# Performance work log

Measured on AMD Instinct MI355X. Metric: run time of the kernel, lower is better.

Reference implementation:

```python
import jax, jax.numpy as jnp
import numpy as np

B, S, T = 256, 1024, 64

def setup_inputs() -> dict:
    key = jax.random.key(0)
    k1, k2, k3, k4, k5 = jax.random.split(key, 5)
    emissions = jax.random.normal(k1, (B, S, T), dtype=jnp.float32)
    tags = jax.random.randint(k2, (B, S), 0, T, dtype=jnp.int64)
    mask = jnp.ones((B, S), dtype=jnp.int32)
    transitions = jax.random.normal(k3, (T, T), dtype=jnp.float32) * 0.1
    start_transitions = jax.random.normal(k4, (T,), dtype=jnp.float32) * 0.1
    end_transitions = jax.random.normal(k5, (T,), dtype=jnp.float32) * 0.1
    return {"emissions": emissions, "tags": tags, "mask": mask,
            "transitions": transitions, "start_transitions": start_transitions,
            "end_transitions": end_transitions}


def _gold_score(emissions, tags, maskf, transitions, start_transitions, end_transitions):
    # emission score at each gold tag: [B, S]
    emit = jnp.take_along_axis(emissions, tags[:, :, None], axis=2)[:, :, 0]
    # transition score between consecutive gold tags: [B, S-1]
    trans = transitions[tags[:, :-1], tags[:, 1:]]
    score = start_transitions[tags[:, 0]] + emit[:, 0]
    score = score + jnp.sum((trans + emit[:, 1:]) * maskf[:, 1:], axis=1)
    last_pos = maskf.astype(jnp.int32).sum(axis=1) - 1           # [B]
    last_tags = jnp.take_along_axis(tags, last_pos[:, None], axis=1)[:, 0]
    return score + end_transitions[last_tags]


def _log_partition(emissions, maskf, transitions, start_transitions, end_transitions):
    alpha0 = start_transitions[None, :] + emissions[:, 0]        # [B, T]

    def step(alpha, xs):
        emit_t, m_t = xs                                         # [B, T], [B]
        # scores[b, i, j] = alpha[b, i] + transitions[i, j] + emit_t[b, j]
        scores = alpha[:, :, None] + transitions[None, :, :] + emit_t[:, None, :]
        new_alpha = jax.nn.logsumexp(scores, axis=1)             # [B, T]
        alpha = jnp.where(m_t[:, None] > 0, new_alpha, alpha)
        return alpha, None

    xs = (jnp.swapaxes(emissions[:, 1:], 0, 1), jnp.swapaxes(maskf[:, 1:], 0, 1))
    alpha, _ = jax.lax.scan(step, alpha0, xs)
    return jax.nn.logsumexp(alpha + end_transitions[None, :], axis=1)  # [B]


def reference(emissions, tags, mask, transitions, start_transitions, end_transitions):
    maskf = mask.astype(emissions.dtype)
    log_Z = _log_partition(emissions, maskf, transitions, start_transitions, end_transitions)
    score = _gold_score(emissions, tags, maskf, transitions, start_transitions, end_transitions)
    return jnp.mean(log_Z - score)
```

## Files before the change

### kernel.cpp

```cpp
#include <hip/hip_runtime.h>

#define Bn 256
#define Sn 1024
#define Tn 64
#define NCH 16
#define BURN 64
#define SLAB 4
#define RAWSTR 260
#define CROW 72
#define MROW 129
#define LN2 0.69314718055994531f
#define L7LN2 4.8520302639196169f

typedef __attribute__((ext_vector_type(8))) short short8;
typedef __attribute__((ext_vector_type(4))) float f32x4;

__device__ __forceinline__ unsigned short f2bf_rne(float f) {
  unsigned u = __float_as_uint(f);
  u = (u + 0x7fffu + ((u >> 16) & 1u)) >> 16;
  return (unsigned short)u;
}
__device__ __forceinline__ unsigned pk2(float hi, float lo) {
  return __builtin_amdgcn_perm(__float_as_uint(hi), __float_as_uint(lo), 0x07060302);
}
__device__ __forceinline__ unsigned pke(float a, float b) {
  return (unsigned)f2bf_rne(__expf(a - L7LN2)) |
         ((unsigned)f2bf_rne(__expf(b - L7LN2)) << 16);
}
__device__ __forceinline__ short8 cat4(uint2 a, uint2 b) {
  union { unsigned u[4]; short8 s; } x;
  x.u[0] = a.x; x.u[1] = a.y; x.u[2] = b.x; x.u[3] = b.y;
  return x.s;
}
__device__ __forceinline__ void gl_lds16(const void* src, void* dst) {
  __builtin_amdgcn_global_load_lds(
      (const __attribute__((address_space(1))) void*)src,
      (__attribute__((address_space(3))) void*)dst, 16, 0, 0);
}
__device__ __forceinline__ void gl_lds4(const void* src, void* dst) {
  __builtin_amdgcn_global_load_lds(
      (const __attribute__((address_space(1))) void*)src,
      (__attribute__((address_space(3))) void*)dst, 4, 0, 0);
}

__global__ __launch_bounds__(256, 1) void crf_scan(
    const float* __restrict__ em, const int* __restrict__ tags,
    const int* __restrict__ mask, const float* __restrict__ trans,
    const float* __restrict__ startt, const float* __restrict__ endt,
    float* __restrict__ wsL, float* __restrict__ wsGold,
    int* __restrict__ wsM, float* __restrict__ wsSE, float* __restrict__ wsA,
    int* __restrict__ cnt, float* __restrict__ out) {
  const int g = blockIdx.x & 15;
  const int c = blockIdx.x >> 4;
  const int Wc = (c == 0) ? 0 : BURN;
  const int Lc = (c == NCH - 1) ? 63 : 64;
  const int TOT = Wc + Lc;
  const int NSLAB = (TOT + SLAB - 1) / SLAB;
  const int t0 = 64 * c + 1;
  const int tstart = t0 - Wc;
  const int tid = threadIdx.x;
  const int wid = tid >> 6;
  const int lane = tid & 63;
  const int m = lane & 15;
  const int q = lane >> 4;
  const int mrow = 8 * (m >> 2) + (m & 3);

  __shared__ __align__(16) float rawS[4][16 * RAWSTR];
  __shared__ __align__(16) short convS[2][SLAB * 16 * CROW];
  __shared__ int maskL[16 * MROW];
  __shared__ int lastF;
  __shared__ float eend[64];
  __shared__ float rsum[4];

  short8 a00, a01, a10, a11, a20, a21, a30, a31;
  uint2 st0, st1, st2, st3;
  float Slog = 0.f;
  int K = 0, NL = 0;
  const f32x4 zero4 = {0.f, 0.f, 0.f, 0.f};

  auto issue_rows = [&](int s, int mm0, int mm1) {
    if (s >= NSLAB) return;
    float* dstb = rawS[s & 3];
    const int rem = TOT - 4 * s;
    if (rem >= SLAB) {
      for (int mm = mm0; mm < mm1; ++mm)
        gl_lds16(em + ((size_t)(16 * g + mm) * Sn + tstart + 4 * s) * 64 + lane * 4,
                 dstb + mm * RAWSTR);
    } else {
      for (int mm = mm0; mm < mm1; ++mm)
        for (int u = 0; u < rem; ++u)
          gl_lds4(em + ((size_t)(16 * g + mm) * Sn + tstart + 4 * s + u) * 64 + lane,
                  dstb + mm * RAWSTR + u * 64);
    }
  };
  auto conv_u = [&](const float* rp, short* cb, int mm, int base, int u) {
    float4 v0 = *(const float4*)(rp + u * 64 + 0);
    float4 v1 = *(const float4*)(rp + u * 64 + 4);
    float4 v2 = *(const float4*)(rp + u * 64 + 8);
    float4 v3 = *(const float4*)(rp + u * 64 + 12);
    uint4 o0, o1;
    o0.x = pke(v0.x, v0.y); o0.y = pke(v0.z, v0.w);
    o1.x = pke(v1.x, v1.y); o1.y = pke(v1.z, v1.w);
    o0.z = pke(v2.x, v2.y); o0.w = pke(v2.z, v2.w);
    o1.z = pke(v3.x, v3.y); o1.w = pke(v3.z, v3.w);
    short* cw = cb + (u * 16 + mm) * CROW + base;
    *(uint4*)(cw) = o0;
    *(uint4*)(cw + 16) = o1;
  };
  auto convert2 = [&](int s, int ua) {
    if (s >= NSLAB) return;
    const int mm = lane & 15, seg = lane >> 4;
    const float* rp = rawS[s & 3] + mm * RAWSTR + seg * 16;
    short* cb = convS[s & 1];
    const int base = (seg >> 1) * 32 + (seg & 1) * 8;
    conv_u(rp, cb, mm, base, ua);
    conv_u(rp, cb, mm, base, ua + 1);
  };

  if (wid == 0) {
#define LOADA(tm, kc, dst) { \
    _Pragma("unroll") for (int jj = 0; jj < 8; ++jj) { \
      int kk = kc * 32 + q * 8 + jj; \
      dst[jj] = (short)f2bf_rne(__expf(trans[kk * Tn + (32 * ((tm) >> 1) + 4 * ((tm) & 1) + mrow)])); \
    } }
    LOADA(0, 0, a00) LOADA(0, 1, a01) LOADA(1, 0, a10) LOADA(1, 1, a11)
    LOADA(2, 0, a20) LOADA(2, 1, a21) LOADA(3, 0, a30) LOADA(3, 1, a31)
#undef LOADA
    if (c == 0) {
#define INIT0(off, ss) { \
      float4 sv = *(const float4*)(startt + (off)); \
      float4 ev = *(const float4*)(em + (size_t)(16 * g + m) * Sn * Tn + (off)); \
      ss.x = (unsigned)f2bf_rne(__expf(sv.x + ev.x)) | \
             ((unsigned)f2bf_rne(__expf(sv.y + ev.y)) << 16); \
      ss.y = (unsigned)f2bf_rne(__expf(sv.z + ev.z)) | \
             ((unsigned)f2bf_rne(__expf(sv.w + ev.w)) << 16); }
      INIT0(8 * q, st0) INIT0(8 * q + 4, st1)
      INIT0(32 + 8 * q, st2) INIT0(36 + 8 * q, st3)
#undef INIT0
    } else {
      st0.x = 0x3F803F80u; st0.y = 0x3F803F80u; st1 = st0; st2 = st0; st3 = st0;
    }
  } else if (wid == 1) {
    issue_rows(0, 0, 6); issue_rows(1, 0, 6); issue_rows(2, 0, 6);
    asm volatile("s_waitcnt vmcnt(0)" ::: "memory");
  } else if (wid == 2) {
    issue_rows(0, 6, 12); issue_rows(1, 6, 12); issue_rows(2, 6, 12);
    const int bm = 16 * g + m;
    const int* tg = tags + (size_t)bm * Sn;
    const int* mkb = mask + (size_t)bm * Sn;
    const float* emb = em + (size_t)bm * Sn * Tn;
    float acc = 0.f;
    int cntg = 0;
    #pragma unroll 4
    for (int i = 0; i < 16; ++i) {
      int t = t0 + q + 4 * i;
      bool ok = t < t0 + Lc;
      int ts = ok ? t : t0;
      int mv = mkb[ts];
      int tp = tg[ts - 1], tc = tg[ts];
      float w = trans[tp * Tn + tc] + emb[(size_t)ts * Tn + tc];
      acc += (ok && mv) ? w : 0.f;
      cntg += ok ? mv : 0;
    }
    acc += __shfl_xor(acc, 16); acc += __shfl_xor(acc, 32);
    cntg += __shfl_xor(cntg, 16); cntg += __shfl_xor(cntg, 32);
    if (q == 0) { wsGold[c * 256 + bm] = acc; wsM[c * 256 + bm] = cntg; }
    asm volatile("s_waitcnt vmcnt(0)" ::: "memory");
  } else {
    issue_rows(0, 12, 16); issue_rows(1, 12, 16); issue_rows(2, 12, 16);
    for (int mm = 0; mm < 16; ++mm) {
      gl_lds4(mask + (size_t)(16 * g + mm) * Sn + tstart + lane,
              (void*)(maskL + mm * MROW));
      bool special = (c == NCH - 1) && (g == 15) && (mm == 15);
      if (!special)
        gl_lds4(mask + (size_t)(16 * g + mm) * Sn + tstart + 64 + lane,
                (void*)(maskL + mm * MROW + 64));
    }
    if (c == NCH - 1 && g == 15) {
      int t = tstart + 64 + lane;
      if (t < Sn) maskL[15 * MROW + 64 + lane] = mask[(size_t)255 * Sn + t];
    }
    asm volatile("s_waitcnt vmcnt(0) lgkmcnt(0)" ::: "memory");
  }
  __syncthreads();

  if (wid == 1) convert2(0, 0);
  else if (wid == 2) convert2(0, 2);
  __syncthreads();

#define UNP(ss, x0, x1, x2, x3) \
  x0 = __uint_as_float(ss.x << 16); x1 = __uint_as_float(ss.x & 0xffff0000u); \
  x2 = __uint_as_float(ss.y << 16); x3 = __uint_as_float(ss.y & 0xffff0000u);

  auto renorm = [&](int ttz) {
    float x00, x01, x02, x03, x10, x11, x12, x13;
    float x20, x21, x22, x23, x30, x31, x32, x33;
    UNP(st0, x00, x01, x02, x03) UNP(st1, x10, x11, x12, x13)
    UNP(st2, x20, x21, x22, x23) UNP(st3, x30, x31, x32, x33)
    float sm = (((x00 + x01) + (x02 + x03)) + ((x10 + x11) + (x12 + x13)))
             + (((x20 + x21) + (x22 + x23)) + ((x30 + x31) + (x32 + x33)));
    sm += __shfl_xor(sm, 16); sm += __shfl_xor(sm, 32);
    if (c != 0 && ttz == BURN) { Slog = __logf(sm); K = 0; NL = 0; }
    int k = 127 - (int)((__float_as_uint(sm) >> 23) & 255u);
    float fk = __uint_as_float((unsigned)(127 + k) << 23);
    x00 *= fk; x01 *= fk; x02 *= fk; x03 *= fk;
    x10 *= fk; x11 *= fk; x12 *= fk; x13 *= fk;
    x20 *= fk; x21 *= fk; x22 *= fk; x23 *= fk;
    x30 *= fk; x31 *= fk; x32 *= fk; x33 *= fk;
    st0.x = pk2(x01, x00); st0.y = pk2(x03, x02);
    st1.x = pk2(x11, x10); st1.y = pk2(x13, x12);
    st2.x = pk2(x21, x20); st2.y = pk2(x23, x22);
    st3.x = pk2(x31, x30); st3.y = pk2(x33, x32);
    K += k;
  };

  auto scan_step = [&](const short* ep, int tt) {
    uint2 eu0 = *(const uint2*)(ep + 0 + 4 * q);
    uint2 eu1 = *(const uint2*)(ep + 16 + 4 * q);
    uint2 eu2 = *(const uint2*)(ep + 32 + 4 * q);
    uint2 eu3 = *(const uint2*)(ep + 48 + 4 * q);
    int mv = maskL[m * MROW + tt];
    short8 b0 = cat4(st0, st1);
    short8 b1 = cat4(st2, st3);
    f32x4 d0 = __builtin_amdgcn_mfma_f32_16x16x32_bf16(a00, b0, zero4, 0, 0, 0);
    f32x4 d1 = __builtin_amdgcn_mfma_f32_16x16x32_bf16(a10, b0, zero4, 0, 0, 0);
    f32x4 d2 = __builtin_amdgcn_mfma_f32_16x16x32_bf16(a20, b0, zero4, 0, 0, 0);
    f32x4 d3 = __builtin_amdgcn_mfma_f32_16x16x32_bf16(a30, b0, zero4, 0, 0, 0);
    d0 = __builtin_amdgcn_mfma_f32_16x16x32_bf16(a01, b1, d0, 0, 0, 0);
    d1 = __builtin_amdgcn_mfma_f32_16x16x32_bf16(a11, b1, d1, 0, 0, 0);
    d2 = __builtin_amdgcn_mfma_f32_16x16x32_bf16(a21, b1, d2, 0, 0, 0);
    d3 = __builtin_amdgcn_mfma_f32_16x16x32_bf16(a31, b1, d3, 0, 0, 0);
    const bool live = (mv != 0);
#define EPI(dd, eu, ss) { \
    float e0 = __uint_as_float(eu.x << 16); \
    float e1 = __uint_as_float(eu.x & 0xffff0000u); \
    float e2 = __uint_as_float(eu.y << 16); \
    float e3 = __uint_as_float(eu.y & 0xffff0000u); \
    unsigned nx = pk2(dd[1] * e1, dd[0] * e0); \
    unsigned ny = pk2(dd[3] * e3, dd[2] * e2); \
    ss.x = live ? nx : ss.x; \
    ss.y = live ? ny : ss.y; }
    EPI(d0, eu0, st0) EPI(d1, eu1, st1) EPI(d2, eu2, st2) EPI(d3, eu3, st3)
#undef EPI
    NL += (live && tt >= Wc) ? 1 : 0;
  };

  const int RT = (TOT - 4) >> 2;
  for (int r = 0; r < NSLAB; ++r) {
    if (wid == 0) {
      if ((r & 1) == 0) renorm(4 * r);
      const short* cbase = convS[r & 1];
      if (r < RT) {
        #pragma unroll
        for (int u = 0; u < SLAB; ++u)
          scan_step(cbase + (u * 16 + m) * CROW, 4 * r + u);
      } else {
        #pragma unroll
        for (int u = 0; u < SLAB; ++u)
          if (4 * r + u < TOT)
            scan_step(cbase + (u * 16 + m) * CROW, 4 * r + u);
      }
    } else if (wid == 1) {
      issue_rows(r + 3, 0, 6);
      convert2(r + 1, 0);
      asm volatile("s_waitcnt lgkmcnt(0)" ::: "memory");
      if (r + 4 < NSLAB) asm volatile("s_waitcnt vmcnt(6)" ::: "memory");
      else               asm volatile("s_waitcnt vmcnt(0)" ::: "memory");
    } else if (wid == 2) {
      issue_rows(r + 3, 6, 12);
      convert2(r + 1, 2);
      asm volatile("s_waitcnt lgkmcnt(0)" ::: "memory");
      if (r + 4 < NSLAB) asm volatile("s_waitcnt vmcnt(6)" ::: "memory");
      else               asm volatile("s_waitcnt vmcnt(0)" ::: "memory");
    } else {
      issue_rows(r + 3, 12, 16);
      if (r + 4 < NSLAB) asm volatile("s_waitcnt vmcnt(4)" ::: "memory");
      else               asm volatile("s_waitcnt vmcnt(0)" ::: "memory");
    }
    __builtin_amdgcn_s_barrier();
    asm volatile("" ::: "memory");
  }

  if (wid == 0) {
    float x00, x01, x02, x03, x10, x11, x12, x13;
    float x20, x21, x22, x23, x30, x31, x32, x33;
    UNP(st0, x00, x01, x02, x03) UNP(st1, x10, x11, x12, x13)
    UNP(st2, x20, x21, x22, x23) UNP(st3, x30, x31, x32, x33)
    float sm = (((x00 + x01) + (x02 + x03)) + ((x10 + x11) + (x12 + x13)))
             + (((x20 + x21) + (x22 + x23)) + ((x30 + x31) + (x32 + x33)));
    sm += __shfl_xor(sm, 16); sm += __shfl_xor(sm, 32);
    const int bm = 16 * g + m;
    float L = __logf(sm) - Slog + LN2 * (float)(7 * NL - K);
    if (q == 0) wsL[c * 256 + bm] = L;
    if (c == NCH - 1) {
      if (q == 0) wsSE[bm] = __logf(sm);
      wsA[(8 * q + 0) * 256 + bm] = x00;  wsA[(8 * q + 1) * 256 + bm] = x01;
      wsA[(8 * q + 2) * 256 + bm] = x02;  wsA[(8 * q + 3) * 256 + bm] = x03;
      wsA[(8 * q + 4) * 256 + bm] = x10;  wsA[(8 * q + 5) * 256 + bm] = x11;
      wsA[(8 * q + 6) * 256 + bm] = x12;  wsA[(8 * q + 7) * 256 + bm] = x13;
      wsA[(32 + 8 * q + 0) * 256 + bm] = x20; wsA[(32 + 8 * q + 1) * 256 + bm] = x21;
      wsA[(32 + 8 * q + 2) * 256 + bm] = x22; wsA[(32 + 8 * q + 3) * 256 + bm] = x23;
      wsA[(36 + 8 * q + 0) * 256 + bm] = x30; wsA[(36 + 8 * q + 1) * 256 + bm] = x31;
      wsA[(36 + 8 * q + 2) * 256 + bm] = x32; wsA[(36 + 8 * q + 3) * 256 + bm] = x33;
    }
  }
#undef UNP

  __threadfence();
  __syncthreads();
  if (tid == 0) lastF = (atomicAdd(cnt, 1) == 255) ? 1 : 0;
  __syncthreads();
  if (lastF) {
    __threadfence();
    if (tid < 64) eend[tid] = __expf(endt[tid]);
    __syncthreads();
    float vsum = 0.f;
    for (int bb = tid; bb < Bn; bb += 256) {
      float sumL = 0.f, gold = 0.f;
      int msum = 0;
      #pragma unroll
      for (int cc = 0; cc < NCH; ++cc) {
        sumL += wsL[cc * 256 + bb];
        gold += wsGold[cc * 256 + bb];
        msum += wsM[cc * 256 + bb];
      }
      msum += mask[(size_t)bb * Sn];
      float se = 0.f;
      for (int jj = 0; jj < Tn; ++jj) se += wsA[jj * 256 + bb] * eend[jj];
      float logZ = sumL + __logf(se) - wsSE[bb];
      int tg0 = tags[(size_t)bb * Sn];
      int lastTag = tags[(size_t)bb * Sn + (msum - 1)];
      gold += startt[tg0] + em[(size_t)bb * Sn * Tn + tg0] + endt[lastTag];
      vsum += logZ - gold;
    }
    #pragma unroll
    for (int o = 32; o > 0; o >>= 1) vsum += __shfl_xor(vsum, o, 64);
    if (lane == 0) rsum[wid] = vsum;
    __syncthreads();
    if (tid == 0) out[0] = (rsum[0] + rsum[1] + rsum[2] + rsum[3]) * (1.0f / Bn);
  }
}

extern "C" void kernel_launch(void* const* d_in, const int* in_sizes, int n_in,
                              void* d_out, int out_size, void* d_ws, size_t ws_size,
                              hipStream_t stream) {
  const float* em     = (const float*)d_in[0];
  const int*   tags   = (const int*)d_in[1];
  const int*   mask   = (const int*)d_in[2];
  const float* trans  = (const float*)d_in[3];
  const float* startt = (const float*)d_in[4];
  const float* endt   = (const float*)d_in[5];
  float* out = (float*)d_out;

  float* wsL    = (float*)d_ws;
  float* wsGold = wsL + NCH * 256;
  int*   wsM    = (int*)(wsGold + NCH * 256);
  float* wsSE   = (float*)(wsM + NCH * 256);
  float* wsA    = wsSE + 256;
  int*   cnt    = (int*)(wsA + 64 * 256);

  hipMemsetAsync(cnt, 0, sizeof(int), stream);
  crf_scan<<<256, 256, 0, stream>>>(em, tags, mask, trans, startt, endt,
                                    wsL, wsGold, wsM, wsSE, wsA, cnt, out);
}
```

Measured before the change: 163.9 us.

## Replace global-to-LDS raw staging with register double-buffered emission loads

```diff
diff --git a/kernel.cpp b/kernel.cpp
--- a/kernel.cpp
+++ b/kernel.cpp
@@ -6,7 +6,6 @@
 #define NCH 16
 #define BURN 64
 #define SLAB 4
-#define RAWSTR 260
 #define CROW 72
 #define MROW 129
 #define LN2 0.69314718055994531f
@@ -31,11 +30,6 @@
   union { unsigned u[4]; short8 s; } x;
   x.u[0] = a.x; x.u[1] = a.y; x.u[2] = b.x; x.u[3] = b.y;
   return x.s;
-}
-__device__ __forceinline__ void gl_lds16(const void* src, void* dst) {
-  __builtin_amdgcn_global_load_lds(
-      (const __attribute__((address_space(1))) void*)src,
-      (__attribute__((address_space(3))) void*)dst, 16, 0, 0);
 }
 __device__ __forceinline__ void gl_lds4(const void* src, void* dst) {
   __builtin_amdgcn_global_load_lds(
@@ -65,7 +59,6 @@
   const int q = lane >> 4;
   const int mrow = 8 * (m >> 2) + (m & 3);
 
-  __shared__ __align__(16) float rawS[4][16 * RAWSTR];
   __shared__ __align__(16) short convS[2][SLAB * 16 * CROW];
   __shared__ int maskL[16 * MROW];
   __shared__ int lastF;
@@ -78,44 +71,38 @@
   int K = 0, NL = 0;
   const f32x4 zero4 = {0.f, 0.f, 0.f, 0.f};
 
-  auto issue_rows = [&](int s, int mm0, int mm1) {
-    if (s >= NSLAB) return;
-    float* dstb = rawS[s & 3];
-    const int rem = TOT - 4 * s;
-    if (rem >= SLAB) {
-      for (int mm = mm0; mm < mm1; ++mm)
-        gl_lds16(em + ((size_t)(16 * g + mm) * Sn + tstart + 4 * s) * 64 + lane * 4,
-                 dstb + mm * RAWSTR);
-    } else {
-      for (int mm = mm0; mm < mm1; ++mm)
-        for (int u = 0; u < rem; ++u)
-          gl_lds4(em + ((size_t)(16 * g + mm) * Sn + tstart + 4 * s + u) * 64 + lane,
-                  dstb + mm * RAWSTR + u * 64);
-    }
-  };
-  auto conv_u = [&](const float* rp, short* cb, int mm, int base, int u) {
-    float4 v0 = *(const float4*)(rp + u * 64 + 0);
-    float4 v1 = *(const float4*)(rp + u * 64 + 4);
-    float4 v2 = *(const float4*)(rp + u * 64 + 8);
-    float4 v3 = *(const float4*)(rp + u * 64 + 12);
-    uint4 o0, o1;
-    o0.x = pke(v0.x, v0.y); o0.y = pke(v0.z, v0.w);
-    o1.x = pke(v1.x, v1.y); o1.y = pke(v1.z, v1.w);
-    o0.z = pke(v2.x, v2.y); o0.w = pke(v2.z, v2.w);
-    o1.z = pke(v3.x, v3.y); o1.w = pke(v3.z, v3.w);
-    short* cw = cb + (u * 16 + mm) * CROW + base;
-    *(uint4*)(cw) = o0;
-    *(uint4*)(cw + 16) = o1;
-  };
-  auto convert2 = [&](int s, int ua) {
-    if (s >= NSLAB) return;
-    const int mm = lane & 15, seg = lane >> 4;
-    const float* rp = rawS[s & 3] + mm * RAWSTR + seg * 16;
-    short* cb = convS[s & 1];
-    const int base = (seg >> 1) * 32 + (seg & 1) * 8;
-    conv_u(rp, cb, mm, base, ua);
-    conv_u(rp, cb, mm, base, ua + 1);
-  };
+  const int mm_ = lane & 15, seg_ = lane >> 4;
+  const int base_ = (seg_ >> 1) * 32 + (seg_ & 1) * 8;
+  const size_t rowoff = (size_t)(16 * g + mm_) * Sn;
+  const int ua = (wid == 1) ? 0 : 2;
+  float4 A0, A1, A2, A3, A4, A5, A6, A7;
+  float4 B0, B1, B2, B3, B4, B5, B6, B7;
+
+#define LOADS(P, s) do { if ((s) < NSLAB) { \
+    int ta_ = tstart + 4 * (s) + ua;  int tb_ = ta_ + 1; \
+    ta_ = min(ta_, Sn - 1);  tb_ = min(tb_, Sn - 1);    \
+    const float* pa_ = em + (rowoff + ta_) * 64 + seg_ * 16; \
+    const float* pb_ = em + (rowoff + tb_) * 64 + seg_ * 16; \
+    P##0 = *(const float4*)(pa_);      P##1 = *(const float4*)(pa_ + 4); \
+    P##2 = *(const float4*)(pa_ + 8);  P##3 = *(const float4*)(pa_ + 12); \
+    P##4 = *(const float4*)(pb_);      P##5 = *(const float4*)(pb_ + 4); \
+    P##6 = *(const float4*)(pb_ + 8);  P##7 = *(const float4*)(pb_ + 12); } } while (0)
+
+#define CONVW(P, s) do { if ((s) < NSLAB) { \
+    short* cb_ = convS[(s) & 1]; \
+    uint4 o0_, o1_; \
+    o0_.x = pke((P##0).x, (P##0).y); o0_.y = pke((P##0).z, (P##0).w); \
+    o1_.x = pke((P##1).x, (P##1).y); o1_.y = pke((P##1).z, (P##1).w); \
+    o0_.z = pke((P##2).x, (P##2).y); o0_.w = pke((P##2).z, (P##2).w); \
+    o1_.z = pke((P##3).x, (P##3).y); o1_.w = pke((P##3).z, (P##3).w); \
+    short* cw_ = cb_ + (ua * 16 + mm_) * CROW + base_; \
+    *(uint4*)(cw_) = o0_;  *(uint4*)(cw_ + 16) = o1_; \
+    o0_.x = pke((P##4).x, (P##4).y); o0_.y = pke((P##4).z, (P##4).w); \
+    o1_.x = pke((P##5).x, (P##5).y); o1_.y = pke((P##5).z, (P##5).w); \
+    o0_.z = pke((P##6).x, (P##6).y); o0_.w = pke((P##6).z, (P##6).w); \
+    o1_.z = pke((P##7).x, (P##7).y); o1_.w = pke((P##7).z, (P##7).w); \
+    cw_ = cb_ + ((ua + 1) * 16 + mm_) * CROW + base_; \
+    *(uint4*)(cw_) = o0_;  *(uint4*)(cw_ + 16) = o1_; } } while (0)
 
   if (wid == 0) {
 #define LOADA(tm, kc, dst) { \
@@ -140,34 +127,7 @@
     } else {
       st0.x = 0x3F803F80u; st0.y = 0x3F803F80u; st1 = st0; st2 = st0; st3 = st0;
     }
-  } else if (wid == 1) {
-    issue_rows(0, 0, 6); issue_rows(1, 0, 6); issue_rows(2, 0, 6);
-    asm volatile("s_waitcnt vmcnt(0)" ::: "memory");
-  } else if (wid == 2) {
-    issue_rows(0, 6, 12); issue_rows(1, 6, 12); issue_rows(2, 6, 12);
-    const int bm = 16 * g + m;
-    const int* tg = tags + (size_t)bm * Sn;
-    const int* mkb = mask + (size_t)bm * Sn;
-    const float* emb = em + (size_t)bm * Sn * Tn;
-    float acc = 0.f;
-    int cntg = 0;
-    #pragma unroll 4
-    for (int i = 0; i < 16; ++i) {
-      int t = t0 + q + 4 * i;
-      bool ok = t < t0 + Lc;
-      int ts = ok ? t : t0;
-      int mv = mkb[ts];
-      int tp = tg[ts - 1], tc = tg[ts];
-      float w = trans[tp * Tn + tc] + emb[(size_t)ts * Tn + tc];
-      acc += (ok && mv) ? w : 0.f;
-      cntg += ok ? mv : 0;
-    }
-    acc += __shfl_xor(acc, 16); acc += __shfl_xor(acc, 32);
-    cntg += __shfl_xor(cntg, 16); cntg += __shfl_xor(cntg, 32);
-    if (q == 0) { wsGold[c * 256 + bm] = acc; wsM[c * 256 + bm] = cntg; }
-    asm volatile("s_waitcnt vmcnt(0)" ::: "memory");
-  } else {
-    issue_rows(0, 12, 16); issue_rows(1, 12, 16); issue_rows(2, 12, 16);
+  } else if (wid == 3) {
     for (int mm = 0; mm < 16; ++mm) {
       gl_lds4(mask + (size_t)(16 * g + mm) * Sn + tstart + lane,
               (void*)(maskL + mm * MROW));
@@ -176,17 +136,41 @@
         gl_lds4(mask + (size_t)(16 * g + mm) * Sn + tstart + 64 + lane,
                 (void*)(maskL + mm * MROW + 64));
     }
+    {
+      const int bm = 16 * g + m;
+      const int* tg = tags + (size_t)bm * Sn;
+      const int* mkb = mask + (size_t)bm * Sn;
+      const float* emb = em + (size_t)bm * Sn * Tn;
+      float acc = 0.f;
+      int cntg = 0;
+      #pragma unroll 4
+      for (int i = 0; i < 16; ++i) {
+        int t = t0 + q + 4 * i;
+        bool ok = t < t0 + Lc;
+        int ts = ok ? t : t0;
+        int mv = mkb[ts];
+        int tp = tg[ts - 1], tc = tg[ts];
+        float w = trans[tp * Tn + tc] + emb[(size_t)ts * Tn + tc];
+        acc += (ok && mv) ? w : 0.f;
+        cntg += ok ? mv : 0;
+      }
+      acc += __shfl_xor(acc, 16); acc += __shfl_xor(acc, 32);
+      cntg += __shfl_xor(cntg, 16); cntg += __shfl_xor(cntg, 32);
+      if (q == 0) { wsGold[c * 256 + bm] = acc; wsM[c * 256 + bm] = cntg; }
+    }
     if (c == NCH - 1 && g == 15) {
       int t = tstart + 64 + lane;
       if (t < Sn) maskL[15 * MROW + 64 + lane] = mask[(size_t)255 * Sn + t];
     }
     asm volatile("s_waitcnt vmcnt(0) lgkmcnt(0)" ::: "memory");
+  } else {
+    LOADS(A, 0);
+    LOADS(B, 1);
+    CONVW(A, 0);
+    asm volatile("s_waitcnt lgkmcnt(0)" ::: "memory");
   }
-  __syncthreads();
-
-  if (wid == 1) convert2(0, 0);
-  else if (wid == 2) convert2(0, 2);
-  __syncthreads();
+  __builtin_amdgcn_s_barrier();
+  asm volatile("" ::: "memory");
 
 #define UNP(ss, x0, x1, x2, x3) \
   x0 = __uint_as_float(ss.x << 16); x1 = __uint_as_float(ss.x & 0xffff0000u); \
@@ -260,26 +244,16 @@
           if (4 * r + u < TOT)
             scan_step(cbase + (u * 16 + m) * CROW, 4 * r + u);
       }
-    } else if (wid == 1) {
-      issue_rows(r + 3, 0, 6);
-      convert2(r + 1, 0);
+    } else if (wid == 1 || wid == 2) {
+      if ((r & 1) == 0) { LOADS(A, r + 2); CONVW(B, r + 1); }
+      else              { LOADS(B, r + 2); CONVW(A, r + 1); }
       asm volatile("s_waitcnt lgkmcnt(0)" ::: "memory");
-      if (r + 4 < NSLAB) asm volatile("s_waitcnt vmcnt(6)" ::: "memory");
-      else               asm volatile("s_waitcnt vmcnt(0)" ::: "memory");
-    } else if (wid == 2) {
-      issue_rows(r + 3, 6, 12);
-      convert2(r + 1, 2);
-      asm volatile("s_waitcnt lgkmcnt(0)" ::: "memory");
-      if (r + 4 < NSLAB) asm volatile("s_waitcnt vmcnt(6)" ::: "memory");
-      else               asm volatile("s_waitcnt vmcnt(0)" ::: "memory");
-    } else {
-      issue_rows(r + 3, 12, 16);
-      if (r + 4 < NSLAB) asm volatile("s_waitcnt vmcnt(4)" ::: "memory");
-      else               asm volatile("s_waitcnt vmcnt(0)" ::: "memory");
     }
     __builtin_amdgcn_s_barrier();
     asm volatile("" ::: "memory");
   }
+#undef LOADS
+#undef CONVW
 
   if (wid == 0) {
     float x00, x01, x02, x03, x10, x11, x12, x13;
```

After: 162.9 us. No clear change (-0.6%).
